# Kernel tuning notes

Hardware: AMD Instinct MI355X
Metric: run time of the kernel (lower is better)

The kernel has to match this reference:

```python
import jax, jax.numpy as jnp
import numpy as np

B, S, P = 2, 1024, 1024          # batch, new tokens, start_pos (cached prefix)
E, H, KV, HD = 2048, 32, 8, 64    # embed, heads, kv groups, head_dim
G = H // KV                       # group size = 4
THETA = 500000.0
CTX = P + S                       # cache/context length = 2048


def _rope_tables(start, seqlen):
    inv_freq = 1.0 / (THETA ** (jnp.arange(0, HD, 2, dtype=jnp.float32) / HD))
    pos = jnp.arange(start, start + seqlen, dtype=jnp.float32)
    freqs = jnp.outer(pos, inv_freq)              # [S, HD/2]
    emb = jnp.concatenate([freqs, freqs], axis=-1)  # [S, HD]
    return jnp.cos(emb), jnp.sin(emb)


def setup_inputs() -> dict:
    key = jax.random.key(0)
    ks = jax.random.split(key, 8)
    x = jax.random.normal(ks[0], (B, S, E), dtype=jnp.float32)
    cos1, sin1 = _rope_tables(P, S)
    cos = jnp.broadcast_to(cos1[None], (B, S, HD))
    sin = jnp.broadcast_to(sin1[None], (B, S, HD))
    # causal-with-offset additive mask: query i (global pos P+i) sees key j <= P+i
    qpos = P + jnp.arange(S)[:, None]
    kpos = jnp.arange(CTX)[None, :]
    mask = jnp.where(kpos <= qpos, 0.0, -1e9).astype(jnp.float32)[None, None]  # [1,1,S,CTX]
    cache_k = jax.random.normal(ks[1], (B, KV, CTX, HD), dtype=jnp.float32)
    cache_v = jax.random.normal(ks[2], (B, KV, CTX, HD), dtype=jnp.float32)
    sc = 0.02
    Wq = jax.random.normal(ks[3], (E, E), dtype=jnp.float32) * sc
    Wk = jax.random.normal(ks[4], (KV * HD, E), dtype=jnp.float32) * sc
    Wv = jax.random.normal(ks[5], (KV * HD, E), dtype=jnp.float32) * sc
    Wo = jax.random.normal(ks[6], (E, E), dtype=jnp.float32) * sc
    return {"x": x, "cos": cos, "sin": sin, "mask": mask,
            "cache_k": cache_k, "cache_v": cache_v,
            "Wq": Wq, "Wk": Wk, "Wv": Wv, "Wo": Wo, "start_pos": P}


def _rotate_half(t):
    t1, t2 = t[..., : HD // 2], t[..., HD // 2:]
    return jnp.concatenate([-t2, t1], axis=-1)


def _apply_rope(t, cos, sin):
    # t: [B, nh, S, HD]; cos/sin: [B, S, HD] -> unsqueeze head dim
    c = cos[:, None]
    s = sin[:, None]
    return t * c + _rotate_half(t) * s


def reference(x, cos, sin, mask, cache_k, cache_v, Wq, Wk, Wv, Wo, start_pos):
    b, s, e = x.shape
    q = (x @ Wq.T).reshape(b, s, H, HD).transpose(0, 2, 1, 3)    # [B,H,S,HD]
    k = (x @ Wk.T).reshape(b, s, KV, HD).transpose(0, 2, 1, 3)   # [B,KV,S,HD]
    v = (x @ Wv.T).reshape(b, s, KV, HD).transpose(0, 2, 1, 3)
    q = _apply_rope(q, cos, sin)
    k = _apply_rope(k, cos, sin)
    ck = cache_k.at[:, :, start_pos:start_pos + s].set(k)
    cv = cache_v.at[:, :, start_pos:start_pos + s].set(v)
    keys = ck[:, :, : start_pos + s]      # [B,KV,T,HD]
    vals = cv[:, :, : start_pos + s]
    # GQA without materializing repeated KV: view q as [B,KV,G,S,HD]
    qg = q.reshape(b, KV, G, s, HD)
    scores = jnp.einsum("bkgsh,bkth->bkgst", qg, keys) / jnp.sqrt(jnp.float32(HD))
    scores = scores + mask[:, :, None]    # broadcast mask over group dim
    probs = jax.nn.softmax(scores.astype(jnp.float32), axis=-1).astype(x.dtype)
    out = jnp.einsum("bkgst,bkth->bkgsh", probs, vals)            # [B,KV,G,S,HD]
    out = out.reshape(b, H, s, HD).transpose(0, 2, 1, 3).reshape(b, s, e)
    return out @ Wo.T
```

## Files before the change

kernel.cpp:

```cpp
#include <hip/hip_runtime.h>
#include <cstddef>

#define B   2
#define S   1024
#define PP  1024
#define CTX 2048
#define E   2048
#define H   32
#define KVH 8
#define HD  64
#define GQ  4
#define NQKV 3072

typedef short s4v  __attribute__((ext_vector_type(4)));
typedef short s8v  __attribute__((ext_vector_type(8)));
typedef float f4v  __attribute__((ext_vector_type(4)));

__device__ __forceinline__ short f2bf(float f) {
  union { float f; unsigned u; } v; v.f = f;
  unsigned r = v.u + 0x7fffu + ((v.u >> 16) & 1u);
  return (short)(r >> 16);
}
__device__ __forceinline__ float bf2f(short h) {
  union { unsigned u; float f; } v; v.u = ((unsigned)(unsigned short)h) << 16;
  return v.f;
}

__device__ __forceinline__ void gl_lds16(const void* g, void* l) {
  __builtin_amdgcn_global_load_lds((const __attribute__((address_space(1))) unsigned*)g,
                                   (__attribute__((address_space(3))) unsigned*)l, 16, 0, 0);
}

__global__ __launch_bounds__(256) void prep(const float* __restrict__ x,
                                            const float* __restrict__ Wq,
                                            const float* __restrict__ Wk,
                                            const float* __restrict__ Wv,
                                            const float* __restrict__ Wo,
                                            const float* __restrict__ ck,
                                            const float* __restrict__ cv,
                                            short* __restrict__ xb,
                                            short* __restrict__ wqkv,
                                            short* __restrict__ wob,
                                            short* __restrict__ keys,
                                            short* __restrict__ vt,
                                            float4* __restrict__ outz) {
  __shared__ short Ts[64][72];
  const int blk = blockIdx.x, tid = threadIdx.x;
  if (blk < 7168) {
    const float* s; short* d; int base;
    if (blk < 2048)      { s = x;  d = xb;             base = blk; }
    else if (blk < 4096) { s = Wq; d = wqkv;           base = blk - 2048; }
    else if (blk < 4608) { s = Wk; d = wqkv + 4194304; base = blk - 4096; }
    else if (blk < 5120) { s = Wv; d = wqkv + 5242880; base = blk - 4608; }
    else                 { s = Wo; d = wob;            base = blk - 5120; }
    int i = (base * 256 + tid) * 8;
    float4 a = *(const float4*)&s[i];
    float4 b = *(const float4*)&s[i + 4];
    s8v o;
    o[0]=f2bf(a.x); o[1]=f2bf(a.y); o[2]=f2bf(a.z); o[3]=f2bf(a.w);
    o[4]=f2bf(b.x); o[5]=f2bf(b.y); o[6]=f2bf(b.z); o[7]=f2bf(b.w);
    *(s8v*)&d[i] = o;
  } else if (blk < 7680) {
    int idx = (blk - 7168) * 256 + tid;
    int bkv = idx >> 13;
    int rem = idx & 8191;
    size_t off = (size_t)bkv * (CTX * HD) + (size_t)rem * 8;
    float4 a = *(const float4*)&ck[off];
    float4 b = *(const float4*)&ck[off + 4];
    s8v o;
    o[0]=f2bf(a.x); o[1]=f2bf(a.y); o[2]=f2bf(a.z); o[3]=f2bf(a.w);
    o[4]=f2bf(b.x); o[5]=f2bf(b.y); o[6]=f2bf(b.z); o[7]=f2bf(b.w);
    *(s8v*)&keys[off] = o;
  } else if (blk < 7936) {
    const int blk2 = blk - 7680;
    const int bkv = blk2 >> 4;
    const int p0  = (blk2 & 15) * 64;
    const float* src = cv + (size_t)bkv * CTX * HD + (size_t)p0 * HD;
    {
      int dq = tid & 15, kb = tid >> 4;
      float4 vv[4];
#pragma unroll
      for (int i = 0; i < 4; i++)
        vv[i] = *(const float4*)&src[(size_t)(kb * 4 + i) * HD + dq * 4];
#pragma unroll
      for (int j = 0; j < 4; j++) {
        s4v p;
        p[0]=f2bf(((const float*)&vv[0])[j]); p[1]=f2bf(((const float*)&vv[1])[j]);
        p[2]=f2bf(((const float*)&vv[2])[j]); p[3]=f2bf(((const float*)&vv[3])[j]);
        *(s4v*)&Ts[dq * 4 + j][kb * 4] = p;
      }
    }
    __syncthreads();
    {
      int d = tid >> 2, c = tid & 3;
      short* dst = vt + ((size_t)bkv * HD + d) * CTX + p0 + (c >> 1) * 32 + (c & 1) * 4;
#pragma unroll
      for (int j = 0; j < 4; j++) {
        s4v q4 = *(const s4v*)&Ts[d][c * 16 + j * 4];
        *(s4v*)&dst[j * 8] = q4;
      }
    }
  } else {
    int i0 = (blk - 7936) * 1024 + tid * 4;
#pragma unroll
    for (int j = 0; j < 4; j++) outz[i0 + j] = make_float4(0.f, 0.f, 0.f, 0.f);
  }
}

__global__ __launch_bounds__(256) void qkv_gemm(const short* __restrict__ A,
                                                const short* __restrict__ Bw,
                                                const float* __restrict__ cosb,
                                                const float* __restrict__ sinb,
                                                short* __restrict__ qb,
                                                short* __restrict__ keys,
                                                short* __restrict__ vt) {
  __shared__ short As[2][8192];
  __shared__ short Bs[2][8192];
  const int tid  = threadIdx.x;
  const int wv   = tid >> 6, lane = tid & 63;
  const int wm   = wv & 1, wn = wv >> 1;
  const int n16  = lane & 15, g = lane >> 4;
  const int m0   = blockIdx.y * 128, n0 = blockIdx.x * 128;
  const int K = 2048;

  const int rr = tid >> 3;
  const int cc = ((tid & 7) ^ (rr & 7)) * 8;
  const short* pA = A  + (size_t)(m0 + rr) * K + cc;
  const short* pB = Bw + (size_t)(n0 + rr) * K + cc;

  auto stage = [&](int buf, int kofs) {
#pragma unroll
    for (int st = 0; st < 4; st++) {
      gl_lds16(pA + kofs + (size_t)st * 32 * K, &As[buf][(st * 256 + wv * 64) * 8]);
      gl_lds16(pB + kofs + (size_t)st * 32 * K, &Bs[buf][(st * 256 + wv * 64) * 8]);
    }
  };

  f4v acc[4][4] = {};
  stage(0, 0);
  int cur = 0;
  for (int k0 = 0; k0 < K; k0 += 64) {
    __syncthreads();
    if (k0 + 64 < K) stage(cur ^ 1, k0 + 64);

#pragma unroll
    for (int kk = 0; kk < 2; kk++) {
      s8v af[4], bf[4];
#pragma unroll
      for (int mt = 0; mt < 4; mt++)
        af[mt] = *(const s8v*)&As[cur][(wm * 64 + mt * 16 + n16) * 64 + (((kk << 2) | g) ^ (n16 & 7)) * 8];
#pragma unroll
      for (int nt = 0; nt < 4; nt++)
        bf[nt] = *(const s8v*)&Bs[cur][(wn * 64 + nt * 16 + n16) * 64 + (((kk << 2) | g) ^ (n16 & 7)) * 8];
#pragma unroll
      for (int mt = 0; mt < 4; mt++)
#pragma unroll
        for (int nt = 0; nt < 4; nt++)
          acc[mt][nt] = __builtin_amdgcn_mfma_f32_16x16x32_bf16(af[mt], bf[nt], acc[mt][nt], 0, 0, 0);
    }
    cur ^= 1;
  }

  const int rowb = m0 + wm * 64 + g * 4;
  const int colb = n0 + wn * 64 + n16;
  if (n0 < 2048) {
#pragma unroll
    for (int mt = 0; mt < 4; mt++)
#pragma unroll
      for (int nt = 0; nt < 4; nt++) {
        size_t base = (size_t)(rowb + mt * 16) * E + colb + nt * 16;
#pragma unroll
        for (int r = 0; r < 4; r++)
          qb[base + (size_t)r * E] = f2bf(acc[mt][nt][r]);
      }
  } else if (n0 < 2560) {
    const int kvh = ((n0 - 2048) >> 6) + wn;
#pragma unroll
    for (int mt = 0; mt < 4; mt++) {
      const int row = rowb + mt * 16;
      const int bb = row >> 10, s = row & 1023;
      const float* crow = cosb + ((size_t)bb * S + s) * HD;
      const float* srow = sinb + ((size_t)bb * S + s) * HD;
      const size_t kdst = (((size_t)bb * KVH + kvh) * CTX + PP + s) * HD;
#pragma unroll
      for (int nt = 0; nt < 2; nt++) {
        const int d = n16 + nt * 16;
#pragma unroll
        for (int r = 0; r < 4; r++) {
          float c  = crow[r * HD + d];
          float sn = srow[r * HD + d];
          float k1 = acc[mt][nt][r], k2 = acc[mt][nt + 2][r];
          keys[kdst + (size_t)r * HD + d]      = f2bf(k1 * c - k2 * sn);
          keys[kdst + (size_t)r * HD + d + 32] = f2bf(k2 * c + k1 * sn);
        }
      }
    }
  } else {
    const int b    = m0 >> 10;
    const int head = ((n0 - 2560) >> 6) + wn;
    const int sbase = (m0 - (b << 10)) + wm * 64;
    const size_t vrowb = (size_t)(b * KVH + head) * HD;
#pragma unroll
    for (int mt = 0; mt < 4; mt++) {
      const int pos = PP + sbase + ((mt >> 1) << 5) + ((mt & 1) << 2) + (g << 3);
#pragma unroll
      for (int nt = 0; nt < 4; nt++) {
        const int d = nt * 16 + n16;
        s4v o;
        o[0] = f2bf(acc[mt][nt][0]); o[1] = f2bf(acc[mt][nt][1]);
        o[2] = f2bf(acc[mt][nt][2]); o[3] = f2bf(acc[mt][nt][3]);
        *(s4v*)&vt[(vrowb + d) * CTX + pos] = o;
      }
    }
  }
}

__global__ __launch_bounds__(256) void gemm_bf16_sk(const short* __restrict__ A,
                                                    const short* __restrict__ Bw,
                                                    float* __restrict__ C,
                                                    int M, int N, int K) {
  __shared__ short As[2][8192];
  __shared__ short Bs[2][8192];
  const int tid  = threadIdx.x;
  const int wv   = tid >> 6, lane = tid & 63;
  const int wm   = wv & 1, wn = wv >> 1;
  const int n16  = lane & 15, g = lane >> 4;
  const int m0   = blockIdx.y * 128, n0 = blockIdx.x * 128;
  const int kh   = K >> 1;
  const int kbeg = blockIdx.z * kh;

  const int rr = tid >> 3;
  const int cc = ((tid & 7) ^ (rr & 7)) * 8;
  const short* pA = A  + (size_t)(m0 + rr) * K + kbeg + cc;
  const short* pB = Bw + (size_t)(n0 + rr) * K + kbeg + cc;

  auto stage = [&](int buf, int kofs) {
#pragma unroll
    for (int st = 0; st < 4; st++) {
      gl_lds16(pA + kofs + (size_t)st * 32 * K, &As[buf][(st * 256 + wv * 64) * 8]);
      gl_lds16(pB + kofs + (size_t)st * 32 * K, &Bs[buf][(st * 256 + wv * 64) * 8]);
    }
  };

  f4v acc[4][4] = {};
  stage(0, 0);
  int cur = 0;
  for (int k0 = 0; k0 < kh; k0 += 64) {
    __syncthreads();
    if (k0 + 64 < kh) stage(cur ^ 1, k0 + 64);

#pragma unroll
    for (int kk = 0; kk < 2; kk++) {
      s8v af[4], bf[4];
#pragma unroll
      for (int mt = 0; mt < 4; mt++)
        af[mt] = *(const s8v*)&As[cur][(wm * 64 + mt * 16 + n16) * 64 + (((kk << 2) | g) ^ (n16 & 7)) * 8];
#pragma unroll
      for (int nt = 0; nt < 4; nt++)
        bf[nt] = *(const s8v*)&Bs[cur][(wn * 64 + nt * 16 + n16) * 64 + (((kk << 2) | g) ^ (n16 & 7)) * 8];
#pragma unroll
      for (int mt = 0; mt < 4; mt++)
#pragma unroll
        for (int nt = 0; nt < 4; nt++)
          acc[mt][nt] = __builtin_amdgcn_mfma_f32_16x16x32_bf16(af[mt], bf[nt], acc[mt][nt], 0, 0, 0);
    }
    cur ^= 1;
  }

#pragma unroll
  for (int mt = 0; mt < 4; mt++)
#pragma unroll
    for (int nt = 0; nt < 4; nt++) {
      size_t base = (size_t)(m0 + wm * 64 + mt * 16 + g * 4) * N + n0 + wn * 64 + nt * 16 + n16;
#pragma unroll
      for (int r = 0; r < 4; r++)
        unsafeAtomicAdd(&C[base + (size_t)r * N], acc[mt][nt][r]);
    }
}

__global__ __launch_bounds__(256) void attn_mfma(const short* __restrict__ qb,
                                                 const float* __restrict__ cosb,
                                                 const float* __restrict__ sinb,
                                                 const short* __restrict__ keys,
                                                 const short* __restrict__ valsT,
                                                 short* __restrict__ attn) {
  __shared__ short Ks[4096];
  __shared__ short VTs[4096];

  const int sblk = 15 - (blockIdx.x & 15);
  const int h    = (blockIdx.x >> 4) & (H - 1);
  const int b    = blockIdx.x >> 9;
  const int kv   = h >> 2;
  const int sq0  = sblk * 64;
  const int kend = PP + sq0 + 64;

  const int tid  = threadIdx.x;
  const int w    = tid >> 6;
  const int lane = tid & 63;
  const int n    = lane & 15;
  const int g    = lane >> 4;

  const short* kbase = keys  + ((size_t)b * KVH + kv) * CTX * HD;
  const short* vtb   = valsT + ((size_t)b * KVH + kv) * (size_t)HD * CTX;

  union { s4v h4[2]; s8v v; } qlo, qhi;
  {
    const size_t row = (size_t)b * S + sq0 + w * 16 + n;
    const short* qrow = qb + row * E + h * 64;
    const float* crow = cosb + row * HD;
    const float* srow = sinb + row * HD;
    const float SC = 0.18033688011112042f;
    s8v q0 = *(const s8v*)&qrow[g * 8];
    s8v q1 = *(const s8v*)&qrow[32 + g * 8];
    float cc[8], ss[8];
    *(float4*)&cc[0] = *(const float4*)&crow[g * 8];
    *(float4*)&cc[4] = *(const float4*)&crow[g * 8 + 4];
    *(float4*)&ss[0] = *(const float4*)&srow[g * 8];
    *(float4*)&ss[4] = *(const float4*)&srow[g * 8 + 4];
#pragma unroll
    for (int j = 0; j < 8; j++) {
      float fl = bf2f(q0[j]), fh = bf2f(q1[j]);
      qlo.v[j] = f2bf((fl * cc[j] - fh * ss[j]) * SC);
      qhi.v[j] = f2bf((fh * cc[j] + fl * ss[j]) * SC);
    }
  }

  f4v O[4] = {{0,0,0,0},{0,0,0,0},{0,0,0,0},{0,0,0,0}};
  float la[4] = {0.f, 0.f, 0.f, 0.f};
  const int qp     = PP + sq0 + w * 16 + n;
  const int qmin_w = PP + sq0 + w * 16;

  const int lrow = lane >> 3;
  const int sw   = (lane & 7) ^ lrow;
  const short* kg0 = kbase + (size_t)(w * 8 + lrow) * HD + sw * 8;
  const short* kg1 = kg0 + 32 * HD;
  const short* vg0 = vtb + (size_t)(w * 8 + lrow) * CTX + sw * 8;
  const short* vg1 = vg0 + (size_t)32 * CTX;
  short* kl0 = Ks + w * 512;
  short* kl1 = Ks + 2048 + w * 512;
  short* vl0 = VTs + w * 512;
  short* vl1 = VTs + 2048 + w * 512;

  const int xsl = (g ^ (n & 7)) * 8;

  for (int k0 = 0; k0 < kend; k0 += 64) {
    __syncthreads();
    gl_lds16(kg0 + (size_t)k0 * HD, kl0);
    gl_lds16(kg1 + (size_t)k0 * HD, kl1);
    gl_lds16(vg0 + k0, vl0);
    gl_lds16(vg1 + k0, vl1);
    __syncthreads();

    if (k0 >= qmin_w + 16) continue;

    f4v sc[4];
#pragma unroll
    for (int st = 0; st < 4; st++) {
      const short* krow = &Ks[(st * 16 + n) * 64];
      s8v alo = *(const s8v*)(krow + xsl);
      s8v ahi = *(const s8v*)(krow + (xsl ^ 32));
      f4v z = {0.f, 0.f, 0.f, 0.f};
      z = __builtin_amdgcn_mfma_f32_16x16x32_bf16(alo, qlo.v, z, 0, 0, 0);
      sc[st] = __builtin_amdgcn_mfma_f32_16x16x32_bf16(ahi, qhi.v, z, 0, 0, 0);
    }

    if (k0 + 63 > qmin_w) {
#pragma unroll
      for (int st = 0; st < 4; st++)
#pragma unroll
        for (int r = 0; r < 4; r++) {
          int kpos = k0 + st * 16 + g * 4 + r;
          if (kpos > qp) sc[st][r] = -3e38f;
        }
    }

    union { unsigned u[4]; s8v v; } pb0, pb1;
#pragma unroll
    for (int st = 0; st < 4; st++) {
      float e0 = __builtin_amdgcn_exp2f(sc[st][0]);
      float e1 = __builtin_amdgcn_exp2f(sc[st][1]);
      float e2 = __builtin_amdgcn_exp2f(sc[st][2]);
      float e3 = __builtin_amdgcn_exp2f(sc[st][3]);
      la[0] += e0; la[1] += e1; la[2] += e2; la[3] += e3;
      unsigned w0, w1;
      asm("v_cvt_pk_bf16_f32 %0, %1, %2" : "=v"(w0) : "v"(e0), "v"(e1));
      asm("v_cvt_pk_bf16_f32 %0, %1, %2" : "=v"(w1) : "v"(e2), "v"(e3));
      if (st < 2) { pb0.u[st * 2] = w0; pb0.u[st * 2 + 1] = w1; }
      else        { pb1.u[(st - 2) * 2] = w0; pb1.u[(st - 2) * 2 + 1] = w1; }
    }

#pragma unroll
    for (int dg = 0; dg < 4; dg++) {
      const short* vr = &VTs[(dg * 16 + n) * 64];
      s8v va = *(const s8v*)(vr + xsl);
      s8v vx = *(const s8v*)(vr + (xsl ^ 32));
      O[dg] = __builtin_amdgcn_mfma_f32_16x16x32_bf16(va, pb0.v, O[dg], 0, 0, 0);
      O[dg] = __builtin_amdgcn_mfma_f32_16x16x32_bf16(vx, pb1.v, O[dg], 0, 0, 0);
    }
  }

  float l = (la[0] + la[1]) + (la[2] + la[3]);
  l += __shfl_xor(l, 16);
  l += __shfl_xor(l, 32);
  const float rl = 1.f / l;
  short* orow = attn + ((size_t)b * S + sq0 + w * 16 + n) * E + h * 64;
#pragma unroll
  for (int dg = 0; dg < 4; dg++) {
    s4v o;
    o[0] = f2bf(O[dg][0] * rl); o[1] = f2bf(O[dg][1] * rl);
    o[2] = f2bf(O[dg][2] * rl); o[3] = f2bf(O[dg][3] * rl);
    *(s4v*)&orow[dg * 16 + g * 4] = o;
  }
}

extern "C" void kernel_launch(void* const* d_in, const int* in_sizes, int n_in,
                              void* d_out, int out_size, void* d_ws, size_t ws_size,
                              hipStream_t stream) {
  const float* x       = (const float*)d_in[0];
  const float* cosb    = (const float*)d_in[1];
  const float* sinb    = (const float*)d_in[2];
  const float* cache_k = (const float*)d_in[4];
  const float* cache_v = (const float*)d_in[5];
  const float* Wq      = (const float*)d_in[6];
  const float* Wk      = (const float*)d_in[7];
  const float* Wv      = (const float*)d_in[8];
  const float* Wo      = (const float*)d_in[9];
  float* out = (float*)d_out;

  short* xb    = (short*)d_ws;
  short* wqkv  = xb + 4194304;
  short* wob   = wqkv + 6291456;
  short* keysb = wob + 4194304;
  short* valsT = keysb + 2097152;
  short* aout  = valsT + 2097152;
  short* qb    = aout + 4194304;

  dim3 blk(256);

  prep<<<8960, blk, 0, stream>>>(x, Wq, Wk, Wv, Wo, cache_k, cache_v,
                                 xb, wqkv, wob, keysb, valsT, (float4*)out);

  qkv_gemm<<<dim3(NQKV / 128, (B * S) / 128), blk, 0, stream>>>(xb, wqkv, cosb, sinb,
                                                                qb, keysb, valsT);

  attn_mfma<<<B * H * (S / 64), blk, 0, stream>>>(qb, cosb, sinb, keysb, valsT, aout);

  gemm_bf16_sk<<<dim3(E / 128, (B * S) / 128, 2), blk, 0, stream>>>(aout, wob, out, B * S, E, E);
}
```

Baseline: 259.3 us.

## Split KV range across waves with double-buffered per-wave staging and LDS reduction

The attention kernel now has each wave own all 64 queries of the block and walk a disjoint, interleaved 32-key slice of the KV range. Each wave stages its own K/V tiles into private LDS buffers, double-buffered and synchronised with vmcnt waits instead of block-wide barriers. Partial outputs and row sums are then reduced across the four waves through LDS before normalisation. This removes the per-tile __syncthreads and lets K/V loads overlap compute. In exchange it uses much more LDS (64KB staging) and registers (16 output accumulators plus 4 Q fragments), which may cut occupancy, and it adds a cross-wave reduction epilogue.

```diff
diff --git a/kernel.cpp b/kernel.cpp
--- a/kernel.cpp
+++ b/kernel.cpp
@@ -284,8 +284,8 @@
                                                  const short* __restrict__ keys,
                                                  const short* __restrict__ valsT,
                                                  short* __restrict__ attn) {
-  __shared__ short Ks[4096];
-  __shared__ short VTs[4096];
+  __shared__ short stg[32768];
+  __shared__ float l_lds[4][64];
 
   const int sblk = 15 - (blockIdx.x & 15);
   const int h    = (blockIdx.x >> 4) & (H - 1);
@@ -293,6 +293,7 @@
   const int kv   = h >> 2;
   const int sq0  = sblk * 64;
   const int kend = PP + sq0 + 64;
+  const int qminb = PP + sq0;
 
   const int tid  = threadIdx.x;
   const int w    = tid >> 6;
@@ -303,9 +304,10 @@
   const short* kbase = keys  + ((size_t)b * KVH + kv) * CTX * HD;
   const short* vtb   = valsT + ((size_t)b * KVH + kv) * (size_t)HD * CTX;
 
-  union { s4v h4[2]; s8v v; } qlo, qhi;
-  {
-    const size_t row = (size_t)b * S + sq0 + w * 16 + n;
+  s8v qlo[4], qhi[4];
+#pragma unroll
+  for (int qg = 0; qg < 4; qg++) {
+    const size_t row = (size_t)b * S + sq0 + qg * 16 + n;
     const short* qrow = qb + row * E + h * 64;
     const float* crow = cosb + row * HD;
     const float* srow = sinb + row * HD;
@@ -320,95 +322,150 @@
 #pragma unroll
     for (int j = 0; j < 8; j++) {
       float fl = bf2f(q0[j]), fh = bf2f(q1[j]);
-      qlo.v[j] = f2bf((fl * cc[j] - fh * ss[j]) * SC);
-      qhi.v[j] = f2bf((fh * cc[j] + fl * ss[j]) * SC);
-    }
-  }
-
-  f4v O[4] = {{0,0,0,0},{0,0,0,0},{0,0,0,0},{0,0,0,0}};
+      qlo[qg][j] = f2bf((fl * cc[j] - fh * ss[j]) * SC);
+      qhi[qg][j] = f2bf((fh * cc[j] + fl * ss[j]) * SC);
+    }
+  }
+  __builtin_amdgcn_sched_barrier(0);
+
+  f4v O[4][4] = {};
   float la[4] = {0.f, 0.f, 0.f, 0.f};
-  const int qp     = PP + sq0 + w * 16 + n;
-  const int qmin_w = PP + sq0 + w * 16;
-
-  const int lrow = lane >> 3;
-  const int sw   = (lane & 7) ^ lrow;
-  const short* kg0 = kbase + (size_t)(w * 8 + lrow) * HD + sw * 8;
-  const short* kg1 = kg0 + 32 * HD;
-  const short* vg0 = vtb + (size_t)(w * 8 + lrow) * CTX + sw * 8;
-  const short* vg1 = vg0 + (size_t)32 * CTX;
-  short* kl0 = Ks + w * 512;
-  short* kl1 = Ks + 2048 + w * 512;
-  short* vl0 = VTs + w * 512;
-  short* vl1 = VTs + 2048 + w * 512;
-
-  const int xsl = (g ^ (n & 7)) * 8;
-
-  for (int k0 = 0; k0 < kend; k0 += 64) {
-    __syncthreads();
-    gl_lds16(kg0 + (size_t)k0 * HD, kl0);
-    gl_lds16(kg1 + (size_t)k0 * HD, kl1);
-    gl_lds16(vg0 + k0, vl0);
-    gl_lds16(vg1 + k0, vl1);
-    __syncthreads();
-
-    if (k0 >= qmin_w + 16) continue;
-
-    f4v sc[4];
-#pragma unroll
-    for (int st = 0; st < 4; st++) {
-      const short* krow = &Ks[(st * 16 + n) * 64];
-      s8v alo = *(const s8v*)(krow + xsl);
-      s8v ahi = *(const s8v*)(krow + (xsl ^ 32));
-      f4v z = {0.f, 0.f, 0.f, 0.f};
-      z = __builtin_amdgcn_mfma_f32_16x16x32_bf16(alo, qlo.v, z, 0, 0, 0);
-      sc[st] = __builtin_amdgcn_mfma_f32_16x16x32_bf16(ahi, qhi.v, z, 0, 0, 0);
-    }
-
-    if (k0 + 63 > qmin_w) {
-#pragma unroll
-      for (int st = 0; st < 4; st++)
-#pragma unroll
-        for (int r = 0; r < 4; r++) {
-          int kpos = k0 + st * 16 + g * 4 + r;
-          if (kpos > qp) sc[st][r] = -3e38f;
-        }
-    }
-
-    union { unsigned u[4]; s8v v; } pb0, pb1;
-#pragma unroll
-    for (int st = 0; st < 4; st++) {
-      float e0 = __builtin_amdgcn_exp2f(sc[st][0]);
-      float e1 = __builtin_amdgcn_exp2f(sc[st][1]);
-      float e2 = __builtin_amdgcn_exp2f(sc[st][2]);
-      float e3 = __builtin_amdgcn_exp2f(sc[st][3]);
-      la[0] += e0; la[1] += e1; la[2] += e2; la[3] += e3;
-      unsigned w0, w1;
+
+  const int krj = lane >> 3;
+  const int kcj = ((lane & 7) ^ (krj & 7)) * 8;
+  const short* kg = kbase + (size_t)krj * HD + kcj;
+  const int vrj = lane >> 2;
+  const int vcj = ((lane & 3) ^ (vrj & 3)) * 8;
+  const short* vg = vtb + (size_t)vrj * CTX + vcj;
+  short* const wreg = stg + w * 8192;
+
+  auto stage = [&](int c, int k0) {
+    short* kd = wreg + c * 4096;
+    short* vd = kd + 2048;
+#pragma unroll
+    for (int j = 0; j < 4; j++)
+      gl_lds16(kg + (size_t)(k0 + j * 8) * HD, kd + j * 512);
+#pragma unroll
+    for (int j = 0; j < 4; j++)
+      gl_lds16(vg + (size_t)(j * 16) * CTX + k0, vd + j * 512);
+  };
+
+  const int xk = (g ^ (n & 7)) * 8;
+  const int xv = (g ^ (n & 3)) * 8;
+
+  stage(0, w * 32);
+  int cur = 0;
+  for (int k0 = w * 32; k0 < kend; k0 += 128) {
+    const bool pf = (k0 + 128 < kend);
+    if (pf) stage(cur ^ 1, k0 + 128);
+    if (pf) asm volatile("s_waitcnt vmcnt(8)" ::: "memory");
+    else    asm volatile("s_waitcnt vmcnt(0)" ::: "memory");
+    __builtin_amdgcn_sched_barrier(0);
+
+    const short* kb = wreg + cur * 4096;
+    const short* vb = kb + 2048;
+
+    f4v sc[2][4];
+#pragma unroll
+    for (int st = 0; st < 2; st++) {
+      const short* krow = kb + (st * 16 + n) * 64;
+      s8v alo = *(const s8v*)(krow + xk);
+      s8v ahi = *(const s8v*)(krow + (xk ^ 32));
+#pragma unroll
+      for (int qg = 0; qg < 4; qg++) {
+        f4v z = {0.f, 0.f, 0.f, 0.f};
+        z = __builtin_amdgcn_mfma_f32_16x16x32_bf16(alo, qlo[qg], z, 0, 0, 0);
+        sc[st][qg] = __builtin_amdgcn_mfma_f32_16x16x32_bf16(ahi, qhi[qg], z, 0, 0, 0);
+      }
+    }
+
+    if (k0 + 31 > qminb) {
+#pragma unroll
+      for (int st = 0; st < 2; st++)
+#pragma unroll
+        for (int qg = 0; qg < 4; qg++)
+#pragma unroll
+          for (int r = 0; r < 4; r++) {
+            int kpos = k0 + st * 16 + g * 4 + r;
+            if (kpos > qminb + qg * 16 + n) sc[st][qg][r] = -3e38f;
+          }
+    }
+
+    union pu { unsigned u[4]; s8v v; } pb[4];
+#pragma unroll
+    for (int qg = 0; qg < 4; qg++) {
+      float e0 = __builtin_amdgcn_exp2f(sc[0][qg][0]);
+      float e1 = __builtin_amdgcn_exp2f(sc[0][qg][1]);
+      float e2 = __builtin_amdgcn_exp2f(sc[0][qg][2]);
+      float e3 = __builtin_amdgcn_exp2f(sc[0][qg][3]);
+      float e4 = __builtin_amdgcn_exp2f(sc[1][qg][0]);
+      float e5 = __builtin_amdgcn_exp2f(sc[1][qg][1]);
+      float e6 = __builtin_amdgcn_exp2f(sc[1][qg][2]);
+      float e7 = __builtin_amdgcn_exp2f(sc[1][qg][3]);
+      la[qg] += ((e0 + e1) + (e2 + e3)) + ((e4 + e5) + (e6 + e7));
+      unsigned w0, w1, w2, w3;
       asm("v_cvt_pk_bf16_f32 %0, %1, %2" : "=v"(w0) : "v"(e0), "v"(e1));
       asm("v_cvt_pk_bf16_f32 %0, %1, %2" : "=v"(w1) : "v"(e2), "v"(e3));
-      if (st < 2) { pb0.u[st * 2] = w0; pb0.u[st * 2 + 1] = w1; }
-      else        { pb1.u[(st - 2) * 2] = w0; pb1.u[(st - 2) * 2 + 1] = w1; }
+      asm("v_cvt_pk_bf16_f32 %0, %1, %2" : "=v"(w2) : "v"(e4), "v"(e5));
+      asm("v_cvt_pk_bf16_f32 %0, %1, %2" : "=v"(w3) : "v"(e6), "v"(e7));
+      pb[qg].u[0] = w0; pb[qg].u[1] = w1; pb[qg].u[2] = w2; pb[qg].u[3] = w3;
     }
 
 #pragma unroll
     for (int dg = 0; dg < 4; dg++) {
-      const short* vr = &VTs[(dg * 16 + n) * 64];
-      s8v va = *(const s8v*)(vr + xsl);
-      s8v vx = *(const s8v*)(vr + (xsl ^ 32));
-      O[dg] = __builtin_amdgcn_mfma_f32_16x16x32_bf16(va, pb0.v, O[dg], 0, 0, 0);
-      O[dg] = __builtin_amdgcn_mfma_f32_16x16x32_bf16(vx, pb1.v, O[dg], 0, 0, 0);
-    }
-  }
-
-  float l = (la[0] + la[1]) + (la[2] + la[3]);
-  l += __shfl_xor(l, 16);
-  l += __shfl_xor(l, 32);
-  const float rl = 1.f / l;
-  short* orow = attn + ((size_t)b * S + sq0 + w * 16 + n) * E + h * 64;
+      s8v va = *(const s8v*)(vb + (dg * 16 + n) * 32 + xv);
+#pragma unroll
+      for (int qg = 0; qg < 4; qg++)
+        O[qg][dg] = __builtin_amdgcn_mfma_f32_16x16x32_bf16(va, pb[qg].v, O[qg][dg], 0, 0, 0);
+    }
+    cur ^= 1;
+  }
+
+#pragma unroll
+  for (int qg = 0; qg < 4; qg++) {
+    float l = la[qg];
+    l += __shfl_xor(l, 16);
+    l += __shfl_xor(l, 32);
+    if (g == 0) l_lds[w][qg * 16 + n] = l;
+  }
+  __syncthreads();
+
+  float* mb  = (float*)stg;
+  float* bufA = mb;
+  float* bufB = mb + 4352;
+  if (w < 2) {
+    float* dst = (w == 0) ? bufA : bufB;
+#pragma unroll
+    for (int qg = 0; qg < 4; qg++)
+#pragma unroll
+      for (int dg = 0; dg < 4; dg++)
+        *(f4v*)&dst[(qg * 16 + n) * 68 + dg * 16 + g * 4] = O[qg][dg];
+  }
+  __syncthreads();
+  if (w >= 2) {
+    float* dst = (w == 2) ? bufA : bufB;
+#pragma unroll
+    for (int qg = 0; qg < 4; qg++)
+#pragma unroll
+      for (int dg = 0; dg < 4; dg++) {
+        float* p = &dst[(qg * 16 + n) * 68 + dg * 16 + g * 4];
+        f4v t = *(f4v*)p;
+        t += O[qg][dg];
+        *(f4v*)p = t;
+      }
+  }
+  __syncthreads();
+
+  const int q = w * 16 + n;
+  const float rl = 1.f / (l_lds[0][q] + l_lds[1][q] + l_lds[2][q] + l_lds[3][q]);
+  short* orow = attn + ((size_t)b * S + sq0 + q) * E + h * 64;
 #pragma unroll
   for (int dg = 0; dg < 4; dg++) {
+    f4v a = *(const f4v*)&bufA[q * 68 + dg * 16 + g * 4];
+    f4v c = *(const f4v*)&bufB[q * 68 + dg * 16 + g * 4];
     s4v o;
-    o[0] = f2bf(O[dg][0] * rl); o[1] = f2bf(O[dg][1] * rl);
-    o[2] = f2bf(O[dg][2] * rl); o[3] = f2bf(O[dg][3] * rl);
+    o[0] = f2bf((a[0] + c[0]) * rl); o[1] = f2bf((a[1] + c[1]) * rl);
+    o[2] = f2bf((a[2] + c[2]) * rl); o[3] = f2bf((a[3] + c[3]) * rl);
     *(s4v*)&orow[dg * 16 + g * 4] = o;
   }
 }
```

New measurement: 276.3 us. 6.5% more time.

## Overlap Wo/cache conversion and output zeroing with QKV GEMM; prioritize attention MFMAs

Applied to the files above, without the earlier changes.

The Wo bf16 conversion, key-cache conversion, value-cache transpose and output zeroing move from the prep kernel into extra blocks of the QKV GEMM launch. This lets that memory-bound work run alongside the GEMM tiles instead of before them. The GEMM grid becomes 1D with manual tile indexing. The attention kernel also raises wave priority around its MFMA sections via s_setprio, which may change how waves interleave on a compute unit.

```diff
diff --git a/kernel.cpp b/kernel.cpp
--- a/kernel.cpp
+++ b/kernel.cpp
@@ -35,92 +35,103 @@
                                             const float* __restrict__ Wq,
                                             const float* __restrict__ Wk,
                                             const float* __restrict__ Wv,
-                                            const float* __restrict__ Wo,
-                                            const float* __restrict__ ck,
-                                            const float* __restrict__ cv,
                                             short* __restrict__ xb,
-                                            short* __restrict__ wqkv,
-                                            short* __restrict__ wob,
-                                            short* __restrict__ keys,
-                                            short* __restrict__ vt,
-                                            float4* __restrict__ outz) {
-  __shared__ short Ts[64][72];
+                                            short* __restrict__ wqkv) {
   const int blk = blockIdx.x, tid = threadIdx.x;
-  if (blk < 7168) {
-    const float* s; short* d; int base;
-    if (blk < 2048)      { s = x;  d = xb;             base = blk; }
-    else if (blk < 4096) { s = Wq; d = wqkv;           base = blk - 2048; }
-    else if (blk < 4608) { s = Wk; d = wqkv + 4194304; base = blk - 4096; }
-    else if (blk < 5120) { s = Wv; d = wqkv + 5242880; base = blk - 4608; }
-    else                 { s = Wo; d = wob;            base = blk - 5120; }
-    int i = (base * 256 + tid) * 8;
-    float4 a = *(const float4*)&s[i];
-    float4 b = *(const float4*)&s[i + 4];
-    s8v o;
-    o[0]=f2bf(a.x); o[1]=f2bf(a.y); o[2]=f2bf(a.z); o[3]=f2bf(a.w);
-    o[4]=f2bf(b.x); o[5]=f2bf(b.y); o[6]=f2bf(b.z); o[7]=f2bf(b.w);
-    *(s8v*)&d[i] = o;
-  } else if (blk < 7680) {
-    int idx = (blk - 7168) * 256 + tid;
-    int bkv = idx >> 13;
-    int rem = idx & 8191;
-    size_t off = (size_t)bkv * (CTX * HD) + (size_t)rem * 8;
-    float4 a = *(const float4*)&ck[off];
-    float4 b = *(const float4*)&ck[off + 4];
-    s8v o;
-    o[0]=f2bf(a.x); o[1]=f2bf(a.y); o[2]=f2bf(a.z); o[3]=f2bf(a.w);
-    o[4]=f2bf(b.x); o[5]=f2bf(b.y); o[6]=f2bf(b.z); o[7]=f2bf(b.w);
-    *(s8v*)&keys[off] = o;
-  } else if (blk < 7936) {
-    const int blk2 = blk - 7680;
-    const int bkv = blk2 >> 4;
-    const int p0  = (blk2 & 15) * 64;
-    const float* src = cv + (size_t)bkv * CTX * HD + (size_t)p0 * HD;
-    {
-      int dq = tid & 15, kb = tid >> 4;
-      float4 vv[4];
-#pragma unroll
-      for (int i = 0; i < 4; i++)
-        vv[i] = *(const float4*)&src[(size_t)(kb * 4 + i) * HD + dq * 4];
-#pragma unroll
-      for (int j = 0; j < 4; j++) {
-        s4v p;
-        p[0]=f2bf(((const float*)&vv[0])[j]); p[1]=f2bf(((const float*)&vv[1])[j]);
-        p[2]=f2bf(((const float*)&vv[2])[j]); p[3]=f2bf(((const float*)&vv[3])[j]);
-        *(s4v*)&Ts[dq * 4 + j][kb * 4] = p;
-      }
-    }
-    __syncthreads();
-    {
-      int d = tid >> 2, c = tid & 3;
-      short* dst = vt + ((size_t)bkv * HD + d) * CTX + p0 + (c >> 1) * 32 + (c & 1) * 4;
-#pragma unroll
-      for (int j = 0; j < 4; j++) {
-        s4v q4 = *(const s4v*)&Ts[d][c * 16 + j * 4];
-        *(s4v*)&dst[j * 8] = q4;
-      }
-    }
-  } else {
-    int i0 = (blk - 7936) * 1024 + tid * 4;
-#pragma unroll
-    for (int j = 0; j < 4; j++) outz[i0 + j] = make_float4(0.f, 0.f, 0.f, 0.f);
-  }
+  const float* s; short* d; int base;
+  if (blk < 2048)      { s = x;  d = xb;             base = blk; }
+  else if (blk < 4096) { s = Wq; d = wqkv;           base = blk - 2048; }
+  else if (blk < 4608) { s = Wk; d = wqkv + 4194304; base = blk - 4096; }
+  else                 { s = Wv; d = wqkv + 5242880; base = blk - 4608; }
+  int i = (base * 256 + tid) * 8;
+  float4 a = *(const float4*)&s[i];
+  float4 b = *(const float4*)&s[i + 4];
+  s8v o;
+  o[0]=f2bf(a.x); o[1]=f2bf(a.y); o[2]=f2bf(a.z); o[3]=f2bf(a.w);
+  o[4]=f2bf(b.x); o[5]=f2bf(b.y); o[6]=f2bf(b.z); o[7]=f2bf(b.w);
+  *(s8v*)&d[i] = o;
 }
 
 __global__ __launch_bounds__(256) void qkv_gemm(const short* __restrict__ A,
                                                 const short* __restrict__ Bw,
                                                 const float* __restrict__ cosb,
                                                 const float* __restrict__ sinb,
+                                                const float* __restrict__ Wo,
+                                                const float* __restrict__ ck,
+                                                const float* __restrict__ cv,
                                                 short* __restrict__ qb,
                                                 short* __restrict__ keys,
-                                                short* __restrict__ vt) {
+                                                short* __restrict__ vt,
+                                                short* __restrict__ wob,
+                                                float4* __restrict__ outz) {
   __shared__ short As[2][8192];
   __shared__ short Bs[2][8192];
-  const int tid  = threadIdx.x;
+  const int tid = threadIdx.x;
+  const int id  = blockIdx.x;
+
+  if (id >= 384) {
+    const int aux = id - 384;
+    if (aux < 2048) {
+      int i = (aux * 256 + tid) * 8;
+      float4 a = *(const float4*)&Wo[i];
+      float4 b = *(const float4*)&Wo[i + 4];
+      s8v o;
+      o[0]=f2bf(a.x); o[1]=f2bf(a.y); o[2]=f2bf(a.z); o[3]=f2bf(a.w);
+      o[4]=f2bf(b.x); o[5]=f2bf(b.y); o[6]=f2bf(b.z); o[7]=f2bf(b.w);
+      *(s8v*)&wob[i] = o;
+    } else if (aux < 2560) {
+      int idx = (aux - 2048) * 256 + tid;
+      int bkv = idx >> 13;
+      int rem = idx & 8191;
+      size_t off = (size_t)bkv * (CTX * HD) + (size_t)rem * 8;
+      float4 a = *(const float4*)&ck[off];
+      float4 b = *(const float4*)&ck[off + 4];
+      s8v o;
+      o[0]=f2bf(a.x); o[1]=f2bf(a.y); o[2]=f2bf(a.z); o[3]=f2bf(a.w);
+      o[4]=f2bf(b.x); o[5]=f2bf(b.y); o[6]=f2bf(b.z); o[7]=f2bf(b.w);
+      *(s8v*)&keys[off] = o;
+    } else if (aux < 2816) {
+      short (*Ts)[72] = (short (*)[72])&As[0][0];
+      const int blk2 = aux - 2560;
+      const int bkv = blk2 >> 4;
+      const int p0  = (blk2 & 15) * 64;
+      const float* src = cv + (size_t)bkv * CTX * HD + (size_t)p0 * HD;
+      {
+        int dq = tid & 15, kb = tid >> 4;
+        float4 vv[4];
+#pragma unroll
+        for (int i = 0; i < 4; i++)
+          vv[i] = *(const float4*)&src[(size_t)(kb * 4 + i) * HD + dq * 4];
+#pragma unroll
+        for (int j = 0; j < 4; j++) {
+          s4v p;
+          p[0]=f2bf(((const float*)&vv[0])[j]); p[1]=f2bf(((const float*)&vv[1])[j]);
+          p[2]=f2bf(((const float*)&vv[2])[j]); p[3]=f2bf(((const float*)&vv[3])[j]);
+          *(s4v*)&Ts[dq * 4 + j][kb * 4] = p;
+        }
+      }
+      __syncthreads();
+      {
+        int d = tid >> 2, c = tid & 3;
+        short* dst = vt + ((size_t)bkv * HD + d) * CTX + p0 + (c >> 1) * 32 + (c & 1) * 4;
+#pragma unroll
+        for (int j = 0; j < 4; j++) {
+          s4v q4 = *(const s4v*)&Ts[d][c * 16 + j * 4];
+          *(s4v*)&dst[j * 8] = q4;
+        }
+      }
+    } else {
+      int i0 = (aux - 2816) * 1024 + tid * 4;
+#pragma unroll
+      for (int j = 0; j < 4; j++) outz[i0 + j] = make_float4(0.f, 0.f, 0.f, 0.f);
+    }
+    return;
+  }
+
   const int wv   = tid >> 6, lane = tid & 63;
   const int wm   = wv & 1, wn = wv >> 1;
   const int n16  = lane & 15, g = lane >> 4;
-  const int m0   = blockIdx.y * 128, n0 = blockIdx.x * 128;
+  const int m0   = (id / 24) * 128, n0 = (id % 24) * 128;
   const int K = 2048;
 
   const int rr = tid >> 3;
@@ -354,6 +365,7 @@
     if (k0 >= qmin_w + 16) continue;
 
     f4v sc[4];
+    __builtin_amdgcn_s_setprio(1);
 #pragma unroll
     for (int st = 0; st < 4; st++) {
       const short* krow = &Ks[(st * 16 + n) * 64];
@@ -363,6 +375,7 @@
       z = __builtin_amdgcn_mfma_f32_16x16x32_bf16(alo, qlo.v, z, 0, 0, 0);
       sc[st] = __builtin_amdgcn_mfma_f32_16x16x32_bf16(ahi, qhi.v, z, 0, 0, 0);
     }
+    __builtin_amdgcn_s_setprio(0);
 
     if (k0 + 63 > qmin_w) {
 #pragma unroll
@@ -389,6 +402,7 @@
       else        { pb1.u[(st - 2) * 2] = w0; pb1.u[(st - 2) * 2 + 1] = w1; }
     }
 
+    __builtin_amdgcn_s_setprio(1);
 #pragma unroll
     for (int dg = 0; dg < 4; dg++) {
       const short* vr = &VTs[(dg * 16 + n) * 64];
@@ -397,6 +411,7 @@
       O[dg] = __builtin_amdgcn_mfma_f32_16x16x32_bf16(va, pb0.v, O[dg], 0, 0, 0);
       O[dg] = __builtin_amdgcn_mfma_f32_16x16x32_bf16(vx, pb1.v, O[dg], 0, 0, 0);
     }
+    __builtin_amdgcn_s_setprio(0);
   }
 
   float l = (la[0] + la[1]) + (la[2] + la[3]);
@@ -437,11 +452,10 @@
 
   dim3 blk(256);
 
-  prep<<<8960, blk, 0, stream>>>(x, Wq, Wk, Wv, Wo, cache_k, cache_v,
-                                 xb, wqkv, wob, keysb, valsT, (float4*)out);
-
-  qkv_gemm<<<dim3(NQKV / 128, (B * S) / 128), blk, 0, stream>>>(xb, wqkv, cosb, sinb,
-                                                                qb, keysb, valsT);
+  prep<<<5120, blk, 0, stream>>>(x, Wq, Wk, Wv, xb, wqkv);
+
+  qkv_gemm<<<4224, blk, 0, stream>>>(xb, wqkv, cosb, sinb, Wo, cache_k, cache_v,
+                                     qb, keysb, valsT, wob, (float4*)out);
 
   attn_mfma<<<B * H * (S / 64), blk, 0, stream>>>(qb, cosb, sinb, keysb, valsT, aout);
 
```

Result: faster. 253.0 us (-2.5%).
